# Kernel tuning notes

Measured on AMD Instinct MI355X. Metric: run time of the kernel, lower is better.

The kernel has to match this reference:

```python
import jax, jax.numpy as jnp
import numpy as np

BS, N, IN_NF, H, EH, OUT_NF, L = 16, 128, 64, 256, 128, 64, 4
C = 1.0


def _lin(k, fan_in, fan_out):
    s = 1.0 / np.sqrt(fan_in)
    return jax.random.uniform(k, (fan_in, fan_out), minval=-s, maxval=s, dtype=jnp.float32)


def setup_inputs() -> dict:
    key = jax.random.key(0)
    ks = jax.random.split(key, 8)
    # fully-connected directed edges (i != j), offset per graph in the batch
    r = np.repeat(np.arange(N), N)
    c = np.tile(np.arange(N), N)
    m = r != c
    r, c = r[m], c[m]  # [N*(N-1)]
    off = (np.arange(BS) * N)[:, None]
    rows = jnp.asarray((r[None, :] + off).reshape(-1), dtype=jnp.int32)  # [BS*N*(N-1)]
    cols = jnp.asarray((c[None, :] + off).reshape(-1), dtype=jnp.int32)

    def stack(kb, fan_in, fan_out):
        return jnp.stack([_lin(jax.random.fold_in(kb, l), fan_in, fan_out) for l in range(L)])

    return {
        "h": jax.random.normal(ks[0], (BS, N, IN_NF), dtype=jnp.float32),
        "rows": rows,
        "cols": cols,
        "w_in": _lin(ks[1], IN_NF, H), "b_in": jnp.zeros((H,), jnp.float32),
        "w_out": _lin(ks[2], H, OUT_NF), "b_out": jnp.zeros((OUT_NF,), jnp.float32),
        "we1": stack(ks[3], 2 * H, EH), "be1": jnp.zeros((L, EH), jnp.float32),
        "we2": stack(ks[4], EH, EH), "be2": jnp.zeros((L, EH), jnp.float32),
        "wn1": stack(ks[5], H + EH, H), "bn1": jnp.zeros((L, H), jnp.float32),
        "wn2": stack(ks[6], H, H), "bn2": jnp.zeros((L, H), jnp.float32),
    }


def reference(h, rows, cols, w_in, b_in, w_out, b_out,
              we1, be1, we2, be2, wn1, bn1, wn2, bn2):
    bs, n, _ = h.shape
    ntot = bs * n
    x = h.reshape(ntot, -1) @ w_in + b_in  # embedding_in -> [ntot, H]
    for l in range(L):  # stacked GCL layers (small fixed count)
        # edge model: gather endpoints, MLP on concatenated pair features
        m = jnp.concatenate([x[rows], x[cols]], axis=-1)        # [E, 2H]
        m = jax.nn.silu(m @ we1[l] + be1[l])                     # [E, EH]
        m = jax.nn.silu(m @ we2[l] + be2[l])                     # [E, EH]
        # node model: scatter-sum messages back to receiver nodes
        agg = jax.ops.segment_sum(m, rows, num_segments=ntot) * C  # [ntot, EH]
        u = jnp.concatenate([x, agg], axis=-1)                   # [ntot, H+EH]
        u = jax.nn.silu(u @ wn1[l] + bn1[l])
        u = u @ wn2[l] + bn2[l]
        x = x + u  # residual
    return x @ w_out + b_out  # embedding_out -> [ntot, OUT_NF]
```

## Files before the change

### kernel.cpp

```cpp
#include <hip/hip_runtime.h>

#define NTOT 2048
#define INF 64
#define HD 256
#define EHD 128
#define ONF 64
#define NL 4

typedef __attribute__((ext_vector_type(8))) short bf16x8;
typedef __attribute__((ext_vector_type(4))) float f32x4;

__device__ __forceinline__ float silu_f(float v) {
    return v * __builtin_amdgcn_rcpf(1.0f + __expf(-v));
}

__device__ __forceinline__ unsigned short f2bf_rn(float f) {
    unsigned u = __float_as_uint(f);
    u += 0x7FFFu + ((u >> 16) & 1u);
    return (unsigned short)(u >> 16);
}
__device__ __forceinline__ void split_rn(float v, unsigned short& h, unsigned short& l) {
    h = f2bf_rn(v);
    l = f2bf_rn(v - __uint_as_float((unsigned)h << 16));
}
__device__ __forceinline__ void split_tr(float v, unsigned& uh, unsigned& ul) {
    unsigned u = __float_as_uint(v);
    uh = u & 0xffff0000u;
    ul = __float_as_uint(v - __uint_as_float(uh)) & 0xffff0000u;
}
__device__ __forceinline__ float bfraw2f(unsigned short s) {
    return __uint_as_float((unsigned)s << 16);
}

__global__ __launch_bounds__(256) void k_prep(
        const float* __restrict__ w_in, const float* __restrict__ we1,
        const float* __restrict__ wn1, const float* __restrict__ wn2,
        const float* __restrict__ w_out, const float* __restrict__ we2,
        short* __restrict__ hwin, short* __restrict__ lwin,
        short* __restrict__ hwe1, short* __restrict__ lwe1,
        short* __restrict__ hwn1, short* __restrict__ lwn1,
        short* __restrict__ hwn2, short* __restrict__ lwn2,
        short* __restrict__ hwout, short* __restrict__ lwout,
        short* __restrict__ hwe2, short* __restrict__ lwe2) {
    const int gid = blockIdx.x * 256 + threadIdx.x;
    const float* src; short* hd; short* ld;
    int sl, dst, KS, N, mode;
    if (gid < 2048)        { sl = gid;                dst = gid;           src = w_in;                                  hd = hwin;  ld = lwin;  KS = 2;  N = 256; mode = 0; }
    else if (gid < 34816)  { int g = gid - 2048;      sl = g & 8191;  dst = g; src = we1 + (size_t)(g >> 13) * 512 * 128;   hd = hwe1;  ld = lwe1;  KS = 8;  N = 256; mode = 1; }
    else if (gid < 83968)  { int g = gid - 34816;     sl = g % 12288; dst = g; src = wn1 + (size_t)(g / 12288) * 384 * 256; hd = hwn1;  ld = lwn1;  KS = 12; N = 256; mode = 0; }
    else if (gid < 116736) { int g = gid - 83968;     sl = g & 8191;  dst = g; src = wn2 + (size_t)(g >> 13) * 256 * 256;   hd = hwn2;  ld = lwn2;  KS = 8;  N = 256; mode = 0; }
    else if (gid < 118784) { int g = gid - 116736;    sl = g;         dst = g; src = w_out;                                 hd = hwout; ld = lwout; KS = 8;  N = 64;  mode = 0; }
    else if (gid < 126976) { int g = gid - 118784;    sl = g & 2047;  dst = g; src = we2 + (size_t)(g >> 11) * 128 * 128;   hd = hwe2;  ld = lwe2;  KS = 4;  N = 128; mode = 0; }
    else return;
    const int lane = sl & 63;
    const int t2 = sl >> 6;
    const int ks = t2 % KS;
    const int nt = t2 / KS;
    const int n = nt * 16 + (lane & 15);
    const int k0 = ks * 32 + ((lane >> 4) << 3);
    short h8[8], l8[8];
#pragma unroll
    for (int i = 0; i < 8; ++i) {
        int k = k0 + i;
        float f;
        if (mode == 1) f = (n < 128) ? src[(size_t)k * 128 + n] : src[(size_t)(256 + k) * 128 + (n - 128)];
        else           f = src[(size_t)k * N + n];
        unsigned short hh, ll;
        split_rn(f, hh, ll);
        h8[i] = (short)hh; l8[i] = (short)ll;
    }
#pragma unroll
    for (int i = 0; i < 8; ++i) {
        hd[(size_t)dst * 8 + i] = h8[i];
        ld[(size_t)dst * 8 + i] = l8[i];
    }
}

__global__ __launch_bounds__(1024, 4) void k_embed_ab(
        const float* __restrict__ h, const float* __restrict__ b_in,
        const float* __restrict__ be1,
        const short* __restrict__ hwin, const short* __restrict__ lwin,
        const short* __restrict__ hwe1, const short* __restrict__ lwe1,
        short* __restrict__ xs_hi, short* __restrict__ xs_lo,
        float* __restrict__ A, float* __restrict__ Bb) {
    __shared__ __align__(16) short hls[2][2][64][8];
    __shared__ __align__(16) short xls[2][8][64][8];
    const int t = threadIdx.x;
    const int mt = blockIdx.x;
    const int n0 = mt * 16;
    const int w = t >> 6, lane = t & 63;
    const int r0 = (lane >> 4) * 4;

    {
        const int m = t >> 6, k = t & 63;
        float v = h[(size_t)(n0 + m) * INF + k];
        unsigned uh, ul;
        split_tr(v, uh, ul);
        const int ks = k >> 5;
        const int lane2 = m + 16 * ((k & 31) >> 3);
        const int i0 = k & 7;
        hls[0][ks][lane2][i0] = (short)(uh >> 16);
        hls[1][ks][lane2][i0] = (short)(ul >> 16);
    }
    __syncthreads();
    f32x4 acc = {0.f, 0.f, 0.f, 0.f};
#pragma unroll
    for (int ks = 0; ks < 2; ++ks) {
        bf16x8 ah = *(const bf16x8*)&hls[0][ks][lane][0];
        bf16x8 al = *(const bf16x8*)&hls[1][ks][lane][0];
        bf16x8 bh = ((const bf16x8*)hwin)[(w * 2 + ks) * 64 + lane];
        bf16x8 bl = ((const bf16x8*)lwin)[(w * 2 + ks) * 64 + lane];
        acc = __builtin_amdgcn_mfma_f32_16x16x32_bf16(ah, bh, acc, 0, 0, 0);
        acc = __builtin_amdgcn_mfma_f32_16x16x32_bf16(al, bh, acc, 0, 0, 0);
        acc = __builtin_amdgcn_mfma_f32_16x16x32_bf16(ah, bl, acc, 0, 0, 0);
    }
    {
        int col = w * 16 + (lane & 15);
        float bias = b_in[col];
        int ks = col >> 5, l2b = 16 * ((col & 31) >> 3), i2 = col & 7;
#pragma unroll
        for (int reg = 0; reg < 4; ++reg) {
            float xv = acc[reg] + bias;
            unsigned uh, ul;
            split_tr(xv, uh, ul);
            xls[0][ks][r0 + reg + l2b][i2] = (short)(uh >> 16);
            xls[1][ks][r0 + reg + l2b][i2] = (short)(ul >> 16);
        }
    }
    __syncthreads();
    {
        int s = t;
        int plane = s >> 9, ks = (s >> 6) & 7, ln = s & 63;
        bf16x8 v = *(const bf16x8*)&xls[plane][ks][ln][0];
        bf16x8* dstp = (bf16x8*)(plane ? xs_lo : xs_hi);
        dstp[(size_t)(mt * 8 + ks) * 64 + ln] = v;
    }
    f32x4 acc1 = {0.f, 0.f, 0.f, 0.f};
#pragma unroll
    for (int ks = 0; ks < 8; ++ks) {
        bf16x8 ah = *(const bf16x8*)&xls[0][ks][lane][0];
        bf16x8 al = *(const bf16x8*)&xls[1][ks][lane][0];
        bf16x8 bh = ((const bf16x8*)hwe1)[(w * 8 + ks) * 64 + lane];
        bf16x8 bl = ((const bf16x8*)lwe1)[(w * 8 + ks) * 64 + lane];
        acc1 = __builtin_amdgcn_mfma_f32_16x16x32_bf16(ah, bh, acc1, 0, 0, 0);
        acc1 = __builtin_amdgcn_mfma_f32_16x16x32_bf16(al, bh, acc1, 0, 0, 0);
        acc1 = __builtin_amdgcn_mfma_f32_16x16x32_bf16(ah, bl, acc1, 0, 0, 0);
    }
    {
        int j = w * 16 + (lane & 15);
        float bias = (j < 128) ? be1[j] : 0.0f;
        float* dstp = (j < 128) ? A : Bb;
        int jj = j & 127;
#pragma unroll
        for (int reg = 0; reg < 4; ++reg) {
            int node = n0 + r0 + reg;
            dstp[(size_t)node * 128 + jj] = acc1[reg] + bias;
        }
    }
}

__global__ __launch_bounds__(256, 4) void k_edge_mfma(
        const float* __restrict__ A, const float* __restrict__ Bb,
        const short* __restrict__ hwe2,
        const float* __restrict__ be2, float* __restrict__ agg) {
    __shared__ __align__(16) short fr[2][4][64][8];
    const int n = blockIdx.x;
    const int b0 = n & ~127;
    const int r = n & 127;
    const int t = threadIdx.x;
    const int w = t >> 6;
    const int lane = t & 63;
    const int kg = t & 15;
    const int ksw = kg >> 2;
    const int lanef = ((kg & 3) << 4);

    float a8[8];
    {
        const float4 a0 = *(const float4*)&A[(size_t)n * EHD + kg * 8];
        const float4 a1 = *(const float4*)&A[(size_t)n * EHD + kg * 8 + 4];
        a8[0] = a0.x; a8[1] = a0.y; a8[2] = a0.z; a8[3] = a0.w;
        a8[4] = a1.x; a8[5] = a1.y; a8[6] = a1.z; a8[7] = a1.w;
    }
    bf16x8 bh[2][4];
#pragma unroll
    for (int nti = 0; nti < 2; ++nti) {
        const int nt = w * 2 + nti;
#pragma unroll
        for (int ks = 0; ks < 4; ++ks)
            bh[nti][ks] = ((const bf16x8*)hwe2)[(nt * 4 + ks) * 64 + lane];
    }
    float be2v[2];
#pragma unroll
    for (int nti = 0; nti < 2; ++nti)
        be2v[nti] = be2[(w * 2 + nti) * 16 + (lane & 15)];

    float colsum[2] = {0.0f, 0.0f};

    for (int ch = 0; ch < 4; ++ch) {
        __syncthreads();
#pragma unroll
        for (int iter = 0; iter < 2; ++iter) {
            const int c_l = iter * 16 + (t >> 4);
            const int mtl = c_l >> 4;
            const float* Brow = &Bb[(size_t)(b0 + ch * 32 + c_l) * EHD + kg * 8];
            const float4 bv0 = *(const float4*)Brow;
            const float4 bv1 = *(const float4*)(Brow + 4);
            float v[8] = {bv0.x + a8[0], bv0.y + a8[1], bv0.z + a8[2], bv0.w + a8[3],
                          bv1.x + a8[4], bv1.y + a8[5], bv1.z + a8[6], bv1.w + a8[7]};
            unsigned short rb[8];
#pragma unroll
            for (int i = 0; i < 8; ++i)
                rb[i] = f2bf_rn(silu_f(v[i]));
            uint4 ph;
            ph.x = (unsigned)rb[0] | ((unsigned)rb[1] << 16);
            ph.y = (unsigned)rb[2] | ((unsigned)rb[3] << 16);
            ph.z = (unsigned)rb[4] | ((unsigned)rb[5] << 16);
            ph.w = (unsigned)rb[6] | ((unsigned)rb[7] << 16);
            const int lf = lanef + (c_l & 15);
            *(uint4*)&fr[mtl][ksw][lf][0] = ph;
        }
        __syncthreads();
#pragma unroll
        for (int mtl = 0; mtl < 2; ++mtl) {
            bf16x8 ah[4];
#pragma unroll
            for (int ks = 0; ks < 4; ++ks)
                ah[ks] = *(const bf16x8*)&fr[mtl][ks][lane][0];
#pragma unroll
            for (int nti = 0; nti < 2; ++nti) {
                f32x4 acc = {0.0f, 0.0f, 0.0f, 0.0f};
#pragma unroll
                for (int ks = 0; ks < 4; ++ks)
                    acc = __builtin_amdgcn_mfma_f32_16x16x32_bf16(ah[ks], bh[nti][ks], acc, 0, 0, 0);
                const int cbase = ch * 32 + mtl * 16 + ((lane >> 4) << 2);
#pragma unroll
                for (int reg = 0; reg < 4; ++reg) {
                    const int c = cbase + reg;
                    float s = silu_f(acc[reg] + be2v[nti]);
                    if (c != r) colsum[nti] += s;
                }
            }
        }
    }
#pragma unroll
    for (int nti = 0; nti < 2; ++nti) {
        float s = colsum[nti];
        s += __shfl_xor(s, 16);
        s += __shfl_xor(s, 32);
        if (lane < 16)
            agg[(size_t)n * EHD + (w * 2 + nti) * 16 + lane] = s;
    }
}

__global__ __launch_bounds__(1024, 4) void k_node_ab(
        const float* __restrict__ agg,
        const float* __restrict__ bn1, const float* __restrict__ bn2,
        const float* __restrict__ be1, const float* __restrict__ b_out,
        const short* __restrict__ hwn1, const short* __restrict__ lwn1,
        const short* __restrict__ hwn2, const short* __restrict__ lwn2,
        const short* __restrict__ hwe1, const short* __restrict__ lwe1,
        const short* __restrict__ hwout, const short* __restrict__ lwout,
        short* __restrict__ xs_hi, short* __restrict__ xs_lo,
        float* __restrict__ A, float* __restrict__ Bb,
        float* __restrict__ outp, int last) {
    __shared__ __align__(16) short cat[2][12][64][8];
    __shared__ __align__(16) short u1[2][8][64][8];
    __shared__ __align__(16) short xn[2][8][64][8];
    const int t = threadIdx.x;
    const int mt = blockIdx.x;
    const int n0 = mt * 16;
    const int w = t >> 6, lane = t & 63;
    const int r0 = (lane >> 4) * 4;

    {
        int s = t;
        int plane = s >> 9, ks = (s >> 6) & 7, ln = s & 63;
        const bf16x8* srcp = (const bf16x8*)(plane ? xs_lo : xs_hi);
        bf16x8 v = srcp[(size_t)(mt * 8 + ks) * 64 + ln];
        *(bf16x8*)&cat[plane][ks][ln][0] = v;
    }
    {
        const int m = t >> 6;
        const int kq = t & 63;
        const int k0 = kq * 2;
        const float2 v2 = *(const float2*)&agg[(size_t)(n0 + m) * EHD + k0];
        unsigned uh0, ul0, uh1, ul1;
        split_tr(v2.x, uh0, ul0);
        split_tr(v2.y, uh1, ul1);
        const int ks = 8 + (k0 >> 5);
        const int lane2 = m + 16 * ((k0 & 31) >> 3);
        const int i0 = k0 & 7;
        *(unsigned*)&cat[0][ks][lane2][i0] = (uh0 >> 16) | uh1;
        *(unsigned*)&cat[1][ks][lane2][i0] = (ul0 >> 16) | ul1;
    }
    __syncthreads();
    f32x4 acc = {0.f, 0.f, 0.f, 0.f};
#pragma unroll
    for (int ks = 0; ks < 12; ++ks) {
        bf16x8 ah = *(const bf16x8*)&cat[0][ks][lane][0];
        bf16x8 al = *(const bf16x8*)&cat[1][ks][lane][0];
        bf16x8 bh = ((const bf16x8*)hwn1)[(w * 12 + ks) * 64 + lane];
        bf16x8 bl = ((const bf16x8*)lwn1)[(w * 12 + ks) * 64 + lane];
        acc = __builtin_amdgcn_mfma_f32_16x16x32_bf16(ah, bh, acc, 0, 0, 0);
        acc = __builtin_amdgcn_mfma_f32_16x16x32_bf16(al, bh, acc, 0, 0, 0);
        acc = __builtin_amdgcn_mfma_f32_16x16x32_bf16(ah, bl, acc, 0, 0, 0);
    }
    const int col = w * 16 + (lane & 15);
    const int ksu = col >> 5, l2b = 16 * ((col & 31) >> 3), i2 = col & 7;
    {
        float bias = bn1[col];
#pragma unroll
        for (int reg = 0; reg < 4; ++reg) {
            float uv = silu_f(acc[reg] + bias);
            unsigned uh, ul;
            split_tr(uv, uh, ul);
            u1[0][ksu][r0 + reg + l2b][i2] = (short)(uh >> 16);
            u1[1][ksu][r0 + reg + l2b][i2] = (short)(ul >> 16);
        }
    }
    __syncthreads();
    f32x4 acc2 = {0.f, 0.f, 0.f, 0.f};
#pragma unroll
    for (int ks = 0; ks < 8; ++ks) {
        bf16x8 ah = *(const bf16x8*)&u1[0][ks][lane][0];
        bf16x8 al = *(const bf16x8*)&u1[1][ks][lane][0];
        bf16x8 bh = ((const bf16x8*)hwn2)[(w * 8 + ks) * 64 + lane];
        bf16x8 bl = ((const bf16x8*)lwn2)[(w * 8 + ks) * 64 + lane];
        acc2 = __builtin_amdgcn_mfma_f32_16x16x32_bf16(ah, bh, acc2, 0, 0, 0);
        acc2 = __builtin_amdgcn_mfma_f32_16x16x32_bf16(al, bh, acc2, 0, 0, 0);
        acc2 = __builtin_amdgcn_mfma_f32_16x16x32_bf16(ah, bl, acc2, 0, 0, 0);
    }
    {
        float bias = bn2[col];
#pragma unroll
        for (int reg = 0; reg < 4; ++reg) {
            int lane2 = r0 + reg + l2b;
            float xold = bfraw2f((unsigned short)cat[0][ksu][lane2][i2])
                       + bfraw2f((unsigned short)cat[1][ksu][lane2][i2]);
            float xv = acc2[reg] + bias + xold;
            unsigned uh, ul;
            split_tr(xv, uh, ul);
            xn[0][ksu][lane2][i2] = (short)(uh >> 16);
            xn[1][ksu][lane2][i2] = (short)(ul >> 16);
        }
    }
    __syncthreads();
    if (!last) {
        {
            int s = t;
            int plane = s >> 9, ks = (s >> 6) & 7, ln = s & 63;
            bf16x8 v = *(const bf16x8*)&xn[plane][ks][ln][0];
            bf16x8* dstp = (bf16x8*)(plane ? xs_lo : xs_hi);
            dstp[(size_t)(mt * 8 + ks) * 64 + ln] = v;
        }
        f32x4 acc3 = {0.f, 0.f, 0.f, 0.f};
#pragma unroll
        for (int ks = 0; ks < 8; ++ks) {
            bf16x8 ah = *(const bf16x8*)&xn[0][ks][lane][0];
            bf16x8 al = *(const bf16x8*)&xn[1][ks][lane][0];
            bf16x8 bh = ((const bf16x8*)hwe1)[(w * 8 + ks) * 64 + lane];
            bf16x8 bl = ((const bf16x8*)lwe1)[(w * 8 + ks) * 64 + lane];
            acc3 = __builtin_amdgcn_mfma_f32_16x16x32_bf16(ah, bh, acc3, 0, 0, 0);
            acc3 = __builtin_amdgcn_mfma_f32_16x16x32_bf16(al, bh, acc3, 0, 0, 0);
            acc3 = __builtin_amdgcn_mfma_f32_16x16x32_bf16(ah, bl, acc3, 0, 0, 0);
        }
        {
            int j = col;
            float bias = (j < 128) ? be1[j] : 0.0f;
            float* dstp = (j < 128) ? A : Bb;
            int jj = j & 127;
#pragma unroll
            for (int reg = 0; reg < 4; ++reg) {
                int node = n0 + r0 + reg;
                dstp[(size_t)node * 128 + jj] = acc3[reg] + bias;
            }
        }
    } else if (w < 4) {
        f32x4 acco = {0.f, 0.f, 0.f, 0.f};
#pragma unroll
        for (int ks = 0; ks < 8; ++ks) {
            bf16x8 ah = *(const bf16x8*)&xn[0][ks][lane][0];
            bf16x8 al = *(const bf16x8*)&xn[1][ks][lane][0];
            bf16x8 bh = ((const bf16x8*)hwout)[(w * 8 + ks) * 64 + lane];
            bf16x8 bl = ((const bf16x8*)lwout)[(w * 8 + ks) * 64 + lane];
            acco = __builtin_amdgcn_mfma_f32_16x16x32_bf16(ah, bh, acco, 0, 0, 0);
            acco = __builtin_amdgcn_mfma_f32_16x16x32_bf16(al, bh, acco, 0, 0, 0);
            acco = __builtin_amdgcn_mfma_f32_16x16x32_bf16(ah, bl, acco, 0, 0, 0);
        }
        float bias = b_out[col];
#pragma unroll
        for (int reg = 0; reg < 4; ++reg) {
            outp[(size_t)(n0 + r0 + reg) * ONF + col] = acco[reg] + bias;
        }
    }
}

extern "C" void kernel_launch(void* const* d_in, const int* in_sizes, int n_in,
                              void* d_out, int out_size, void* d_ws, size_t ws_size,
                              hipStream_t stream) {
    const float* h     = (const float*)d_in[0];
    const float* w_in  = (const float*)d_in[3];
    const float* b_in  = (const float*)d_in[4];
    const float* w_out = (const float*)d_in[5];
    const float* b_out = (const float*)d_in[6];
    const float* we1   = (const float*)d_in[7];
    const float* be1   = (const float*)d_in[8];
    const float* we2   = (const float*)d_in[9];
    const float* be2   = (const float*)d_in[10];
    const float* wn1   = (const float*)d_in[11];
    const float* bn1   = (const float*)d_in[12];
    const float* wn2   = (const float*)d_in[13];
    const float* bn2   = (const float*)d_in[14];

    float* A    = (float*)d_ws;
    float* Bb   = A + 262144;
    float* agg  = Bb + 262144;
    short* xs_hi = (short*)(agg + 262144);
    short* xs_lo = xs_hi + 524288;
    short* hwin  = xs_lo + 524288;
    short* lwin  = hwin + 16384;
    short* hwe1  = lwin + 16384;
    short* lwe1  = hwe1 + 262144;
    short* hwn1  = lwe1 + 262144;
    short* lwn1  = hwn1 + 393216;
    short* hwn2  = lwn1 + 393216;
    short* lwn2  = hwn2 + 262144;
    short* hwout = lwn2 + 262144;
    short* lwout = hwout + 16384;
    short* hwe2  = lwout + 16384;
    short* lwe2  = hwe2 + 65536;
    float* outp  = (float*)d_out;

    k_prep<<<496, 256, 0, stream>>>(w_in, we1, wn1, wn2, w_out, we2,
        hwin, lwin, hwe1, lwe1, hwn1, lwn1, hwn2, lwn2, hwout, lwout, hwe2, lwe2);
    k_embed_ab<<<128, 1024, 0, stream>>>(h, b_in, be1, hwin, lwin, hwe1, lwe1,
        xs_hi, xs_lo, A, Bb);
    for (int l = 0; l < NL; ++l) {
        const int last = (l == NL - 1);
        const int lp = last ? 0 : (l + 1);
        k_edge_mfma<<<NTOT, 256, 0, stream>>>(A, Bb,
            hwe2 + (size_t)l * 2048 * 8,
            be2 + l * EHD, agg);
        k_node_ab<<<128, 1024, 0, stream>>>(agg,
            bn1 + l * HD, bn2 + l * HD, be1 + lp * EHD, b_out,
            hwn1 + (size_t)l * 12288 * 8, lwn1 + (size_t)l * 12288 * 8,
            hwn2 + (size_t)l * 8192 * 8, lwn2 + (size_t)l * 8192 * 8,
            hwe1 + (size_t)lp * 8192 * 8, lwe1 + (size_t)lp * 8192 * 8,
            hwout, lwout, xs_hi, xs_lo, A, Bb, outp, last);
    }
}
```

Before: 170.4 us.

## Double-buffer edge-feature LDS tile and overlap next-chunk prep with MFMA

The edge kernel now keeps two LDS buffers. It loads and SiLU-converts the next 32-column chunk of B while MFMAs run on the current chunk, which removes one barrier per chunk and hides global load latency. MFMA issue is given raised wave priority, and the diagonal mask is applied with a select instead of a branch. The prep kernel also stops writing the unused low-part of we2. The cost is more LDS and more registers per thread, which could reduce occupancy.

```diff
diff --git a/kernel.cpp b/kernel.cpp
--- a/kernel.cpp
+++ b/kernel.cpp
@@ -41,7 +41,7 @@
         short* __restrict__ hwn1, short* __restrict__ lwn1,
         short* __restrict__ hwn2, short* __restrict__ lwn2,
         short* __restrict__ hwout, short* __restrict__ lwout,
-        short* __restrict__ hwe2, short* __restrict__ lwe2) {
+        short* __restrict__ hwe2) {
     const int gid = blockIdx.x * 256 + threadIdx.x;
     const float* src; short* hd; short* ld;
     int sl, dst, KS, N, mode;
@@ -50,7 +50,7 @@
     else if (gid < 83968)  { int g = gid - 34816;     sl = g % 12288; dst = g; src = wn1 + (size_t)(g / 12288) * 384 * 256; hd = hwn1;  ld = lwn1;  KS = 12; N = 256; mode = 0; }
     else if (gid < 116736) { int g = gid - 83968;     sl = g & 8191;  dst = g; src = wn2 + (size_t)(g >> 13) * 256 * 256;   hd = hwn2;  ld = lwn2;  KS = 8;  N = 256; mode = 0; }
     else if (gid < 118784) { int g = gid - 116736;    sl = g;         dst = g; src = w_out;                                 hd = hwout; ld = lwout; KS = 8;  N = 64;  mode = 0; }
-    else if (gid < 126976) { int g = gid - 118784;    sl = g & 2047;  dst = g; src = we2 + (size_t)(g >> 11) * 128 * 128;   hd = hwe2;  ld = lwe2;  KS = 4;  N = 128; mode = 0; }
+    else if (gid < 126976) { int g = gid - 118784;    sl = g & 2047;  dst = g; src = we2 + (size_t)(g >> 11) * 128 * 128;   hd = hwe2;  ld = 0;     KS = 4;  N = 128; mode = 0; }
     else return;
     const int lane = sl & 63;
     const int t2 = sl >> 6;
@@ -70,9 +70,10 @@
         h8[i] = (short)hh; l8[i] = (short)ll;
     }
 #pragma unroll
-    for (int i = 0; i < 8; ++i) {
-        hd[(size_t)dst * 8 + i] = h8[i];
-        ld[(size_t)dst * 8 + i] = l8[i];
+    for (int i = 0; i < 8; ++i) hd[(size_t)dst * 8 + i] = h8[i];
+    if (ld) {
+#pragma unroll
+        for (int i = 0; i < 8; ++i) ld[(size_t)dst * 8 + i] = l8[i];
     }
 }
 
@@ -163,7 +164,7 @@
         const float* __restrict__ A, const float* __restrict__ Bb,
         const short* __restrict__ hwe2,
         const float* __restrict__ be2, float* __restrict__ agg) {
-    __shared__ __align__(16) short fr[2][4][64][8];
+    __shared__ __align__(16) short fr[2][2][4][64][8];
     const int n = blockIdx.x;
     const int b0 = n & ~127;
     const int r = n & 127;
@@ -196,48 +197,85 @@
 
     float colsum[2] = {0.0f, 0.0f};
 
+#pragma unroll
+    for (int iter = 0; iter < 2; ++iter) {
+        const int c_l = iter * 16 + (t >> 4);
+        const int mtl = c_l >> 4;
+        const float* Brow = &Bb[(size_t)(b0 + c_l) * EHD + kg * 8];
+        const float4 bv0 = *(const float4*)Brow;
+        const float4 bv1 = *(const float4*)(Brow + 4);
+        float v[8] = {bv0.x + a8[0], bv0.y + a8[1], bv0.z + a8[2], bv0.w + a8[3],
+                      bv1.x + a8[4], bv1.y + a8[5], bv1.z + a8[6], bv1.w + a8[7]};
+        unsigned short rb[8];
+#pragma unroll
+        for (int i = 0; i < 8; ++i) rb[i] = f2bf_rn(silu_f(v[i]));
+        uint4 ph;
+        ph.x = (unsigned)rb[0] | ((unsigned)rb[1] << 16);
+        ph.y = (unsigned)rb[2] | ((unsigned)rb[3] << 16);
+        ph.z = (unsigned)rb[4] | ((unsigned)rb[5] << 16);
+        ph.w = (unsigned)rb[6] | ((unsigned)rb[7] << 16);
+        *(uint4*)&fr[0][mtl][ksw][lanef + (c_l & 15)][0] = ph;
+    }
+
     for (int ch = 0; ch < 4; ++ch) {
+        const int cur = ch & 1;
         __syncthreads();
-#pragma unroll
-        for (int iter = 0; iter < 2; ++iter) {
-            const int c_l = iter * 16 + (t >> 4);
-            const int mtl = c_l >> 4;
-            const float* Brow = &Bb[(size_t)(b0 + ch * 32 + c_l) * EHD + kg * 8];
-            const float4 bv0 = *(const float4*)Brow;
-            const float4 bv1 = *(const float4*)(Brow + 4);
-            float v[8] = {bv0.x + a8[0], bv0.y + a8[1], bv0.z + a8[2], bv0.w + a8[3],
-                          bv1.x + a8[4], bv1.y + a8[5], bv1.z + a8[6], bv1.w + a8[7]};
-            unsigned short rb[8];
-#pragma unroll
-            for (int i = 0; i < 8; ++i)
-                rb[i] = f2bf_rn(silu_f(v[i]));
-            uint4 ph;
-            ph.x = (unsigned)rb[0] | ((unsigned)rb[1] << 16);
-            ph.y = (unsigned)rb[2] | ((unsigned)rb[3] << 16);
-            ph.z = (unsigned)rb[4] | ((unsigned)rb[5] << 16);
-            ph.w = (unsigned)rb[6] | ((unsigned)rb[7] << 16);
-            const int lf = lanef + (c_l & 15);
-            *(uint4*)&fr[mtl][ksw][lf][0] = ph;
-        }
-        __syncthreads();
+        float nv[2][8];
+        if (ch < 3) {
+#pragma unroll
+            for (int iter = 0; iter < 2; ++iter) {
+                const int c_l = iter * 16 + (t >> 4);
+                const float* Brow = &Bb[(size_t)(b0 + (ch + 1) * 32 + c_l) * EHD + kg * 8];
+                const float4 bv0 = *(const float4*)Brow;
+                const float4 bv1 = *(const float4*)(Brow + 4);
+                nv[iter][0] = bv0.x; nv[iter][1] = bv0.y; nv[iter][2] = bv0.z; nv[iter][3] = bv0.w;
+                nv[iter][4] = bv1.x; nv[iter][5] = bv1.y; nv[iter][6] = bv1.z; nv[iter][7] = bv1.w;
+            }
+        }
+        f32x4 acc[2][2];
+        __builtin_amdgcn_s_setprio(1);
 #pragma unroll
         for (int mtl = 0; mtl < 2; ++mtl) {
             bf16x8 ah[4];
 #pragma unroll
             for (int ks = 0; ks < 4; ++ks)
-                ah[ks] = *(const bf16x8*)&fr[mtl][ks][lane][0];
+                ah[ks] = *(const bf16x8*)&fr[cur][mtl][ks][lane][0];
 #pragma unroll
             for (int nti = 0; nti < 2; ++nti) {
-                f32x4 acc = {0.0f, 0.0f, 0.0f, 0.0f};
+                f32x4 a = {0.0f, 0.0f, 0.0f, 0.0f};
 #pragma unroll
                 for (int ks = 0; ks < 4; ++ks)
-                    acc = __builtin_amdgcn_mfma_f32_16x16x32_bf16(ah[ks], bh[nti][ks], acc, 0, 0, 0);
-                const int cbase = ch * 32 + mtl * 16 + ((lane >> 4) << 2);
+                    a = __builtin_amdgcn_mfma_f32_16x16x32_bf16(ah[ks], bh[nti][ks], a, 0, 0, 0);
+                acc[mtl][nti] = a;
+            }
+        }
+        __builtin_amdgcn_s_setprio(0);
+        if (ch < 3) {
+#pragma unroll
+            for (int iter = 0; iter < 2; ++iter) {
+                const int c_l = iter * 16 + (t >> 4);
+                const int mtl = c_l >> 4;
+                unsigned short rb[8];
+#pragma unroll
+                for (int i = 0; i < 8; ++i) rb[i] = f2bf_rn(silu_f(nv[iter][i] + a8[i]));
+                uint4 ph;
+                ph.x = (unsigned)rb[0] | ((unsigned)rb[1] << 16);
+                ph.y = (unsigned)rb[2] | ((unsigned)rb[3] << 16);
+                ph.z = (unsigned)rb[4] | ((unsigned)rb[5] << 16);
+                ph.w = (unsigned)rb[6] | ((unsigned)rb[7] << 16);
+                *(uint4*)&fr[cur ^ 1][mtl][ksw][lanef + (c_l & 15)][0] = ph;
+            }
+        }
+#pragma unroll
+        for (int mtl = 0; mtl < 2; ++mtl) {
+            const int cbase = ch * 32 + mtl * 16 + ((lane >> 4) << 2);
+#pragma unroll
+            for (int nti = 0; nti < 2; ++nti) {
 #pragma unroll
                 for (int reg = 0; reg < 4; ++reg) {
                     const int c = cbase + reg;
-                    float s = silu_f(acc[reg] + be2v[nti]);
-                    if (c != r) colsum[nti] += s;
+                    float s = silu_f(acc[mtl][nti][reg] + be2v[nti]);
+                    colsum[nti] += (c != r) ? s : 0.0f;
                 }
             }
         }
@@ -428,11 +466,10 @@
     short* hwout = lwn2 + 262144;
     short* lwout = hwout + 16384;
     short* hwe2  = lwout + 16384;
-    short* lwe2  = hwe2 + 65536;
     float* outp  = (float*)d_out;
 
     k_prep<<<496, 256, 0, stream>>>(w_in, we1, wn1, wn2, w_out, we2,
-        hwin, lwin, hwe1, lwe1, hwn1, lwn1, hwn2, lwn2, hwout, lwout, hwe2, lwe2);
+        hwin, lwin, hwe1, lwe1, hwn1, lwn1, hwn2, lwn2, hwout, lwout, hwe2);
     k_embed_ab<<<128, 1024, 0, stream>>>(h, b_in, be1, hwin, lwin, hwe1, lwe1,
         xs_hi, xs_lo, A, Bb);
     for (int l = 0; l < NL; ++l) {
```

Result: faster. 163.6 us (-4.0%).

## Stage all edge features in LDS up front and split columns across two wave halves

Applied to the files above, without the earlier changes.

The edge kernel now uses 512 threads. Each block computes the silu'd pair features for all 128 neighbor columns into a single LDS buffer with one barrier, instead of four chunked load/compute rounds that each need two barriers. The two halves of the waves each take two chunks, and their partial column sums are combined through a small LDS reduction before writing agg. The LDS layout is XOR-swizzled to reduce bank conflicts, and k_prep no longer writes the unused low-part we2 array. The cost is more LDS per block, which may lower occupancy, and an extra barrier for the reduction.

```diff
diff --git a/kernel.cpp b/kernel.cpp
--- a/kernel.cpp
+++ b/kernel.cpp
@@ -41,7 +41,7 @@
         short* __restrict__ hwn1, short* __restrict__ lwn1,
         short* __restrict__ hwn2, short* __restrict__ lwn2,
         short* __restrict__ hwout, short* __restrict__ lwout,
-        short* __restrict__ hwe2, short* __restrict__ lwe2) {
+        short* __restrict__ hwe2) {
     const int gid = blockIdx.x * 256 + threadIdx.x;
     const float* src; short* hd; short* ld;
     int sl, dst, KS, N, mode;
@@ -50,7 +50,7 @@
     else if (gid < 83968)  { int g = gid - 34816;     sl = g % 12288; dst = g; src = wn1 + (size_t)(g / 12288) * 384 * 256; hd = hwn1;  ld = lwn1;  KS = 12; N = 256; mode = 0; }
     else if (gid < 116736) { int g = gid - 83968;     sl = g & 8191;  dst = g; src = wn2 + (size_t)(g >> 13) * 256 * 256;   hd = hwn2;  ld = lwn2;  KS = 8;  N = 256; mode = 0; }
     else if (gid < 118784) { int g = gid - 116736;    sl = g;         dst = g; src = w_out;                                 hd = hwout; ld = lwout; KS = 8;  N = 64;  mode = 0; }
-    else if (gid < 126976) { int g = gid - 118784;    sl = g & 2047;  dst = g; src = we2 + (size_t)(g >> 11) * 128 * 128;   hd = hwe2;  ld = lwe2;  KS = 4;  N = 128; mode = 0; }
+    else if (gid < 126976) { int g = gid - 118784;    sl = g & 2047;  dst = g; src = we2 + (size_t)(g >> 11) * 128 * 128;   hd = hwe2;  ld = 0;     KS = 4;  N = 128; mode = 0; }
     else return;
     const int lane = sl & 63;
     const int t2 = sl >> 6;
@@ -70,9 +70,10 @@
         h8[i] = (short)hh; l8[i] = (short)ll;
     }
 #pragma unroll
-    for (int i = 0; i < 8; ++i) {
-        hd[(size_t)dst * 8 + i] = h8[i];
-        ld[(size_t)dst * 8 + i] = l8[i];
+    for (int i = 0; i < 8; ++i) hd[(size_t)dst * 8 + i] = h8[i];
+    if (ld) {
+#pragma unroll
+        for (int i = 0; i < 8; ++i) ld[(size_t)dst * 8 + i] = l8[i];
     }
 }
 
@@ -159,32 +160,46 @@
     }
 }
 
-__global__ __launch_bounds__(256, 4) void k_edge_mfma(
+__global__ __launch_bounds__(512, 4) void k_edge_mfma(
         const float* __restrict__ A, const float* __restrict__ Bb,
         const short* __restrict__ hwe2,
         const float* __restrict__ be2, float* __restrict__ agg) {
-    __shared__ __align__(16) short fr[2][4][64][8];
+    __shared__ __align__(16) short fr[4][2][4][64][8];
+    __shared__ float red[2][4][2][16];
     const int n = blockIdx.x;
     const int b0 = n & ~127;
     const int r = n & 127;
     const int t = threadIdx.x;
-    const int w = t >> 6;
-    const int lane = t & 63;
-    const int kg = t & 15;
-    const int ksw = kg >> 2;
-    const int lanef = ((kg & 3) << 4);
-
-    float a8[8];
-    {
-        const float4 a0 = *(const float4*)&A[(size_t)n * EHD + kg * 8];
-        const float4 a1 = *(const float4*)&A[(size_t)n * EHD + kg * 8 + 4];
-        a8[0] = a0.x; a8[1] = a0.y; a8[2] = a0.z; a8[3] = a0.w;
-        a8[4] = a1.x; a8[5] = a1.y; a8[6] = a1.z; a8[7] = a1.w;
-    }
+    const int w = t >> 6, lane = t & 63;
+    const int sh = w >> 2, jt = w & 3;
+
+#pragma unroll
+    for (int i = 0; i < 4; ++i) {
+        const int E = i * 512 + t;
+        const int c = E >> 4, ko = E & 15;
+        const int ks = ko >> 2;
+        const float4 bv0 = *(const float4*)&Bb[(size_t)(b0 + c) * EHD + ko * 8];
+        const float4 bv1 = *(const float4*)&Bb[(size_t)(b0 + c) * EHD + ko * 8 + 4];
+        const float4 av0 = *(const float4*)&A[(size_t)n * EHD + ko * 8];
+        const float4 av1 = *(const float4*)&A[(size_t)n * EHD + ko * 8 + 4];
+        float v[8] = {bv0.x + av0.x, bv0.y + av0.y, bv0.z + av0.z, bv0.w + av0.w,
+                      bv1.x + av1.x, bv1.y + av1.y, bv1.z + av1.z, bv1.w + av1.w};
+        unsigned short rb[8];
+#pragma unroll
+        for (int j = 0; j < 8; ++j) rb[j] = f2bf_rn(silu_f(v[j]));
+        uint4 ph;
+        ph.x = (unsigned)rb[0] | ((unsigned)rb[1] << 16);
+        ph.y = (unsigned)rb[2] | ((unsigned)rb[3] << 16);
+        ph.z = (unsigned)rb[4] | ((unsigned)rb[5] << 16);
+        ph.w = (unsigned)rb[6] | ((unsigned)rb[7] << 16);
+        const int lf = (c & 15) | ((ko & 3) << 4);
+        *(uint4*)&fr[c >> 5][(c >> 4) & 1][ks][lf ^ (ks << 1)][0] = ph;
+    }
+
     bf16x8 bh[2][4];
 #pragma unroll
     for (int nti = 0; nti < 2; ++nti) {
-        const int nt = w * 2 + nti;
+        const int nt = jt * 2 + nti;
 #pragma unroll
         for (int ks = 0; ks < 4; ++ks)
             bh[nti][ks] = ((const bf16x8*)hwe2)[(nt * 4 + ks) * 64 + lane];
@@ -192,52 +207,32 @@
     float be2v[2];
 #pragma unroll
     for (int nti = 0; nti < 2; ++nti)
-        be2v[nti] = be2[(w * 2 + nti) * 16 + (lane & 15)];
+        be2v[nti] = be2[(jt * 2 + nti) * 16 + (lane & 15)];
+
+    __syncthreads();
 
     float colsum[2] = {0.0f, 0.0f};
-
-    for (int ch = 0; ch < 4; ++ch) {
-        __syncthreads();
-#pragma unroll
-        for (int iter = 0; iter < 2; ++iter) {
-            const int c_l = iter * 16 + (t >> 4);
-            const int mtl = c_l >> 4;
-            const float* Brow = &Bb[(size_t)(b0 + ch * 32 + c_l) * EHD + kg * 8];
-            const float4 bv0 = *(const float4*)Brow;
-            const float4 bv1 = *(const float4*)(Brow + 4);
-            float v[8] = {bv0.x + a8[0], bv0.y + a8[1], bv0.z + a8[2], bv0.w + a8[3],
-                          bv1.x + a8[4], bv1.y + a8[5], bv1.z + a8[6], bv1.w + a8[7]};
-            unsigned short rb[8];
-#pragma unroll
-            for (int i = 0; i < 8; ++i)
-                rb[i] = f2bf_rn(silu_f(v[i]));
-            uint4 ph;
-            ph.x = (unsigned)rb[0] | ((unsigned)rb[1] << 16);
-            ph.y = (unsigned)rb[2] | ((unsigned)rb[3] << 16);
-            ph.z = (unsigned)rb[4] | ((unsigned)rb[5] << 16);
-            ph.w = (unsigned)rb[6] | ((unsigned)rb[7] << 16);
-            const int lf = lanef + (c_l & 15);
-            *(uint4*)&fr[mtl][ksw][lf][0] = ph;
-        }
-        __syncthreads();
+#pragma unroll
+    for (int chl = 0; chl < 2; ++chl) {
+        const int ch = sh * 2 + chl;
 #pragma unroll
         for (int mtl = 0; mtl < 2; ++mtl) {
             bf16x8 ah[4];
 #pragma unroll
             for (int ks = 0; ks < 4; ++ks)
-                ah[ks] = *(const bf16x8*)&fr[mtl][ks][lane][0];
+                ah[ks] = *(const bf16x8*)&fr[ch][mtl][ks][lane ^ (ks << 1)][0];
+            const int cbase = ch * 32 + mtl * 16 + ((lane >> 4) << 2);
 #pragma unroll
             for (int nti = 0; nti < 2; ++nti) {
-                f32x4 acc = {0.0f, 0.0f, 0.0f, 0.0f};
+                f32x4 a = {0.0f, 0.0f, 0.0f, 0.0f};
 #pragma unroll
                 for (int ks = 0; ks < 4; ++ks)
-                    acc = __builtin_amdgcn_mfma_f32_16x16x32_bf16(ah[ks], bh[nti][ks], acc, 0, 0, 0);
-                const int cbase = ch * 32 + mtl * 16 + ((lane >> 4) << 2);
+                    a = __builtin_amdgcn_mfma_f32_16x16x32_bf16(ah[ks], bh[nti][ks], a, 0, 0, 0);
 #pragma unroll
                 for (int reg = 0; reg < 4; ++reg) {
                     const int c = cbase + reg;
-                    float s = silu_f(acc[reg] + be2v[nti]);
-                    if (c != r) colsum[nti] += s;
+                    float s = silu_f(a[reg] + be2v[nti]);
+                    colsum[nti] += (c != r) ? s : 0.0f;
                 }
             }
         }
@@ -247,8 +242,13 @@
         float s = colsum[nti];
         s += __shfl_xor(s, 16);
         s += __shfl_xor(s, 32);
-        if (lane < 16)
-            agg[(size_t)n * EHD + (w * 2 + nti) * 16 + lane] = s;
+        if (lane < 16) red[sh][jt][nti][lane] = s;
+    }
+    __syncthreads();
+    if (t < 128) {
+        const int jtf = t >> 5, ntif = (t >> 4) & 1, j16 = t & 15;
+        agg[(size_t)n * EHD + jtf * 32 + ntif * 16 + j16] =
+            red[0][jtf][ntif][j16] + red[1][jtf][ntif][j16];
     }
 }
 
@@ -428,17 +428,16 @@
     short* hwout = lwn2 + 262144;
     short* lwout = hwout + 16384;
     short* hwe2  = lwout + 16384;
-    short* lwe2  = hwe2 + 65536;
     float* outp  = (float*)d_out;
 
     k_prep<<<496, 256, 0, stream>>>(w_in, we1, wn1, wn2, w_out, we2,
-        hwin, lwin, hwe1, lwe1, hwn1, lwn1, hwn2, lwn2, hwout, lwout, hwe2, lwe2);
+        hwin, lwin, hwe1, lwe1, hwn1, lwn1, hwn2, lwn2, hwout, lwout, hwe2);
     k_embed_ab<<<128, 1024, 0, stream>>>(h, b_in, be1, hwin, lwin, hwe1, lwe1,
         xs_hi, xs_lo, A, Bb);
     for (int l = 0; l < NL; ++l) {
         const int last = (l == NL - 1);
         const int lp = last ? 0 : (l + 1);
-        k_edge_mfma<<<NTOT, 256, 0, stream>>>(A, Bb,
+        k_edge_mfma<<<NTOT, 512, 0, stream>>>(A, Bb,
             hwe2 + (size_t)l * 2048 * 8,
             be2 + l * EHD, agg);
         k_node_ab<<<128, 1024, 0, stream>>>(agg,
```

Measured after the change: 170.2 us. No clear change (-0.1%).
